# Performance work log

Measured on AMD Instinct MI355X. Metric: run time of the kernel, lower is better.

Reference implementation:

```python
import jax, jax.numpy as jnp
import numpy as np

NUM_HEADS = 16
KEY_DEPTH = 1024


def setup_inputs() -> dict:
    key = jax.random.key(0)
    ks = jax.random.split(key, 7)
    B, L, D = 2, 2048, 1024
    scale = 1.0 / np.sqrt(D)
    return {
        "query_antecedent": jax.random.normal(ks[0], (B, L, D), jnp.float32),
        "memory_antecedent": jax.random.normal(ks[1], (B, L, D), jnp.float32),
        "bias": jax.random.normal(ks[2], (1, 1, L, L), jnp.float32),
        "Wq": jax.random.normal(ks[3], (D, KEY_DEPTH), jnp.float32) * scale,
        "Wk": jax.random.normal(ks[4], (D, KEY_DEPTH), jnp.float32) * scale,
        "Wv": jax.random.normal(ks[5], (D, KEY_DEPTH), jnp.float32) * scale,
        "Wo": jax.random.normal(ks[6], (KEY_DEPTH, D), jnp.float32) * scale,
    }


def _split_heads(x, h):
    # [B, L, D] -> [B, H, L, D/H]
    b, l, d = x.shape
    return x.reshape(b, l, h, d // h).transpose(0, 2, 1, 3)


def reference(query_antecedent, memory_antecedent, bias, Wq, Wk, Wv, Wo):
    h = NUM_HEADS
    d_head = KEY_DEPTH // h
    q = _split_heads(query_antecedent @ Wq, h) * (d_head ** -0.5)
    k = _split_heads(memory_antecedent @ Wk, h)
    v = _split_heads(memory_antecedent @ Wv, h)
    # [B, H, Lq, Lk]
    logits = jnp.einsum("bhqd,bhkd->bhqk", q, k) + bias
    weights = jax.nn.softmax(logits, axis=-1)
    x = jnp.einsum("bhqk,bhkd->bhqd", weights, v)
    # combine heads: [B, H, L, d] -> [B, L, H*d]
    b, _, l, d = x.shape
    x = x.transpose(0, 2, 1, 3).reshape(b, l, h * d)
    return x @ Wo
```

## Files before the change

kernel.cpp:

```cpp
#include <hip/hip_runtime.h>
#include <hip/hip_bf16.h>


typedef __attribute__((ext_vector_type(8))) short short8;
typedef __attribute__((ext_vector_type(4))) short short4v;
typedef __attribute__((ext_vector_type(4))) float float4v;

#define BATCH 2
#define LSEQ 2048
#define DMODEL 1024
#define NHEADS 16
#define DHEAD 64
#define MROWS 4096
#define QKVLD 3072

__global__ __launch_bounds__(256)
void convert_kernel(const float* __restrict__ qa, const float* __restrict__ ma,
                    __hip_bfloat16* __restrict__ qo, __hip_bfloat16* __restrict__ mo)
{
    const size_t i = ((size_t)blockIdx.x * 256 + threadIdx.x) * 8;
    const float* src = blockIdx.y ? ma : qa;
    __hip_bfloat16* dst = blockIdx.y ? mo : qo;
    float4 v0 = *reinterpret_cast<const float4*>(src + i);
    float4 v1 = *reinterpret_cast<const float4*>(src + i + 4);
    union { __hip_bfloat16 h[8]; int4 v; } pk;
    pk.h[0] = (__hip_bfloat16)v0.x; pk.h[1] = (__hip_bfloat16)v0.y;
    pk.h[2] = (__hip_bfloat16)v0.z; pk.h[3] = (__hip_bfloat16)v0.w;
    pk.h[4] = (__hip_bfloat16)v1.x; pk.h[5] = (__hip_bfloat16)v1.y;
    pk.h[6] = (__hip_bfloat16)v1.z; pk.h[7] = (__hip_bfloat16)v1.w;
    *reinterpret_cast<int4*>(dst + i) = pk.v;
}

__global__ __launch_bounds__(256)
void transpose_w_kernel(const float* __restrict__ W0, const float* __restrict__ W1,
                        const float* __restrict__ W2, const float* __restrict__ W3,
                        __hip_bfloat16* __restrict__ T0, __hip_bfloat16* __restrict__ T1,
                        __hip_bfloat16* __restrict__ T2, __hip_bfloat16* __restrict__ T3)
{
    __shared__ __hip_bfloat16 T[64][68];

    const float* W; __hip_bfloat16* D;
    if      (blockIdx.z == 0) { W = W0; D = T0; }
    else if (blockIdx.z == 1) { W = W1; D = T1; }
    else if (blockIdx.z == 2) { W = W2; D = T2; }
    else                      { W = W3; D = T3; }

    const int t  = threadIdx.x;
    const int n0 = blockIdx.x * 64;
    const int k0 = blockIdx.y * 64;

#pragma unroll
    for (int p = 0; p < 4; ++p) {
        const int r = p * 16 + (t >> 4);
        const int c = (t & 15) * 4;
        float4 v = *reinterpret_cast<const float4*>(&W[(size_t)(k0 + r) * DMODEL + n0 + c]);
        union { __hip_bfloat16 h[4]; ushort4 v; } pk;
        pk.h[0] = (__hip_bfloat16)v.x; pk.h[1] = (__hip_bfloat16)v.y;
        pk.h[2] = (__hip_bfloat16)v.z; pk.h[3] = (__hip_bfloat16)v.w;
        *reinterpret_cast<ushort4*>(&T[r][c]) = pk.v;
    }
    __syncthreads();
#pragma unroll
    for (int p = 0; p < 2; ++p) {
        const int n  = p * 32 + (t & 31);
        const int kc = (t >> 5) * 8;
        union { __hip_bfloat16 h[8]; int4 v; } pk;
#pragma unroll
        for (int j = 0; j < 8; ++j) pk.h[j] = T[kc + j][n];
        *reinterpret_cast<int4*>(&D[(size_t)(n0 + n) * DMODEL + k0 + kc]) = pk.v;
    }
}

__global__ __launch_bounds__(256)
void gemm_bt_kernel(const __hip_bfloat16* __restrict__ A0,
                    const __hip_bfloat16* __restrict__ A1, int nsplit,
                    float alpha0, float alpha1,
                    const __hip_bfloat16* __restrict__ Bt,
                    float* __restrict__ Cf, __hip_bfloat16* __restrict__ Cb,
                    int K, int ldc)
{
    __shared__ __hip_bfloat16 As[128][40];
    __shared__ __hip_bfloat16 Bs[128][40];

    const int t    = threadIdx.x;
    const int w    = t >> 6;
    const int lane = t & 63;
    const int l15  = lane & 15;
    const int lq   = lane >> 4;
    const int m0   = blockIdx.y * 128;
    const int n0   = blockIdx.x * 128;
    const int wm   = (w >> 1) * 64;
    const int wn   = (w & 1) * 64;
    const int sr   = t >> 1;
    const int sc   = (t & 1) * 16;

    const __hip_bfloat16* A = (n0 < nsplit) ? A0 : A1;
    const float alpha = (n0 < nsplit) ? alpha0 : alpha1;

    float4v acc[4][4];
#pragma unroll
    for (int mi = 0; mi < 4; ++mi)
#pragma unroll
        for (int ni = 0; ni < 4; ++ni) acc[mi][ni] = (float4v){0.f, 0.f, 0.f, 0.f};

    const __hip_bfloat16* Arow = A  + (size_t)(m0 + sr) * K + sc;
    const __hip_bfloat16* Brow = Bt + (size_t)(n0 + sr) * K + sc;

    int4 a0 = *reinterpret_cast<const int4*>(Arow);
    int4 a1 = *reinterpret_cast<const int4*>(Arow + 8);
    int4 b0 = *reinterpret_cast<const int4*>(Brow);
    int4 b1 = *reinterpret_cast<const int4*>(Brow + 8);

    for (int k0 = 0; k0 < K; k0 += 32) {
        __syncthreads();
        *reinterpret_cast<int4*>(&As[sr][sc])     = a0;
        *reinterpret_cast<int4*>(&As[sr][sc + 8]) = a1;
        *reinterpret_cast<int4*>(&Bs[sr][sc])     = b0;
        *reinterpret_cast<int4*>(&Bs[sr][sc + 8]) = b1;
        const int kn = (k0 + 32 < K) ? k0 + 32 : k0;
        a0 = *reinterpret_cast<const int4*>(Arow + kn);
        a1 = *reinterpret_cast<const int4*>(Arow + kn + 8);
        b0 = *reinterpret_cast<const int4*>(Brow + kn);
        b1 = *reinterpret_cast<const int4*>(Brow + kn + 8);
        __syncthreads();

        short8 af[4], bf[4];
#pragma unroll
        for (int mi = 0; mi < 4; ++mi)
            af[mi] = *reinterpret_cast<const short8*>(&As[wm + mi * 16 + l15][lq * 8]);
#pragma unroll
        for (int ni = 0; ni < 4; ++ni)
            bf[ni] = *reinterpret_cast<const short8*>(&Bs[wn + ni * 16 + l15][lq * 8]);
#pragma unroll
        for (int mi = 0; mi < 4; ++mi)
#pragma unroll
            for (int ni = 0; ni < 4; ++ni)
                acc[mi][ni] = __builtin_amdgcn_mfma_f32_16x16x32_bf16(
                    af[mi], bf[ni], acc[mi][ni], 0, 0, 0);
    }

#pragma unroll
    for (int mi = 0; mi < 4; ++mi)
#pragma unroll
        for (int ni = 0; ni < 4; ++ni)
#pragma unroll
            for (int r = 0; r < 4; ++r) {
                const int row = m0 + wm + mi * 16 + lq * 4 + r;
                const int col = n0 + wn + ni * 16 + l15;
                const float v = acc[mi][ni][r] * alpha;
                if (Cf) Cf[(size_t)row * ldc + col] = v;
                else    Cb[(size_t)row * ldc + col] = (__hip_bfloat16)v;
            }
}

#define KSTR 68
#define PSTR 132

__global__ __launch_bounds__(512, 4)
void attn_mfma_kernel(const __hip_bfloat16* __restrict__ QKV,
                      const float* __restrict__ bias,
                      __hip_bfloat16* __restrict__ X)
{
    __shared__ __hip_bfloat16 Ks[128][KSTR];
    __shared__ __hip_bfloat16 Vt[64][PSTR];

    const int t   = threadIdx.x;
    const int w   = t >> 6;
    const int l15 = t & 15;
    const int lq  = (t & 63) >> 4;

    const int bid = blockIdx.x;
    const int r8  = bid & 7;
    const int j   = bid >> 3;
    const int bh  = r8 + 8 * (j >> 4);
    const int q0  = (j & 15) * 128;
    const int b   = bh >> 4;
    const int h   = bh & 15;

    const __hip_bfloat16* Kb = QKV + (size_t)b * LSEQ * QKVLD + 1024 + h * DHEAD;
    const __hip_bfloat16* Vb = Kb + 1024;

    short8 aq[2];
    {
        const __hip_bfloat16* qrow = QKV +
            (size_t)(b * LSEQ + q0 + w * 16 + l15) * QKVLD + h * DHEAD + lq * 8;
        aq[0] = *reinterpret_cast<const short8*>(qrow);
        aq[1] = *reinterpret_cast<const short8*>(qrow + 32);
    }

    const float* bp = bias + (size_t)(q0 + w * 16 + l15) * LSEQ + lq * 4;

    float lsum = 0.f;
    float4v o_acc[4];
#pragma unroll
    for (int n = 0; n < 4; ++n) o_acc[n] = (float4v){0.f, 0.f, 0.f, 0.f};

    const int skey = t >> 2;
    const int sdh  = (t & 3) * 16;
    const int a    = t & 3;
    const int cblk = ((skey >> 5) << 2) | ((skey >> 2) & 3);
    const int vcol = (((cblk ^ a) << 3)) | ((((skey >> 4) & 1) << 2)) | (skey & 3);

    int4 pk0, pk1, pv0, pv1;
    {
        const __hip_bfloat16* ks = Kb + (size_t)skey * QKVLD + sdh;
        pk0 = *reinterpret_cast<const int4*>(ks);
        pk1 = *reinterpret_cast<const int4*>(ks + 8);
        const __hip_bfloat16* vs = Vb + (size_t)skey * QKVLD + sdh;
        pv0 = *reinterpret_cast<const int4*>(vs);
        pv1 = *reinterpret_cast<const int4*>(vs + 8);
    }

    for (int kt = 0; kt < LSEQ / 128; ++kt) {
        const int k0 = kt * 128;
        __syncthreads();
        *reinterpret_cast<int4*>(&Ks[skey][sdh])     = pk0;
        *reinterpret_cast<int4*>(&Ks[skey][sdh + 8]) = pk1;
        {
            const __hip_bfloat16* vp0 = reinterpret_cast<const __hip_bfloat16*>(&pv0);
            const __hip_bfloat16* vp1 = reinterpret_cast<const __hip_bfloat16*>(&pv1);
#pragma unroll
            for (int jj = 0; jj < 8; ++jj) Vt[sdh + jj][vcol]     = vp0[jj];
#pragma unroll
            for (int jj = 0; jj < 8; ++jj) Vt[sdh + 8 + jj][vcol] = vp1[jj];
        }
        {
            const int knext = (kt + 1 < LSEQ / 128) ? k0 + 128 : k0;
            const __hip_bfloat16* ks = Kb + (size_t)(knext + skey) * QKVLD + sdh;
            pk0 = *reinterpret_cast<const int4*>(ks);
            pk1 = *reinterpret_cast<const int4*>(ks + 8);
            const __hip_bfloat16* vs = Vb + (size_t)(knext + skey) * QKVLD + sdh;
            pv0 = *reinterpret_cast<const int4*>(vs);
            pv1 = *reinterpret_cast<const int4*>(vs + 8);
        }
        __syncthreads();

#pragma unroll
        for (int m = 0; m < 4; ++m) {
            short8 bkA0 = *reinterpret_cast<const short8*>(&Ks[(2*m)    *16 + l15][lq * 8]);
            short8 bkA1 = *reinterpret_cast<const short8*>(&Ks[(2*m)    *16 + l15][32 + lq * 8]);
            short8 bkB0 = *reinterpret_cast<const short8*>(&Ks[(2*m + 1)*16 + l15][lq * 8]);
            short8 bkB1 = *reinterpret_cast<const short8*>(&Ks[(2*m + 1)*16 + l15][32 + lq * 8]);
            float4v bvA = *reinterpret_cast<const float4v*>(bp + k0 + 32 * m);
            float4v bvB = *reinterpret_cast<const float4v*>(bp + k0 + 32 * m + 16);

            float4v sA = (float4v){0.f, 0.f, 0.f, 0.f};
            float4v sB = (float4v){0.f, 0.f, 0.f, 0.f};
            __builtin_amdgcn_s_setprio(1);
            sA = __builtin_amdgcn_mfma_f32_16x16x32_bf16(bkA0, aq[0], sA, 0, 0, 0);
            sA = __builtin_amdgcn_mfma_f32_16x16x32_bf16(bkA1, aq[1], sA, 0, 0, 0);
            sB = __builtin_amdgcn_mfma_f32_16x16x32_bf16(bkB0, aq[0], sB, 0, 0, 0);
            sB = __builtin_amdgcn_mfma_f32_16x16x32_bf16(bkB1, aq[1], sB, 0, 0, 0);
            __builtin_amdgcn_s_setprio(0);

            union { __hip_bfloat16 hh[8]; short8 v; } pp;
#pragma unroll
            for (int r = 0; r < 4; ++r) {
                const float e = __expf(sA[r] + bvA[r]);
                lsum += e;
                pp.hh[r] = (__hip_bfloat16)e;
            }
#pragma unroll
            for (int r = 0; r < 4; ++r) {
                const float e = __expf(sB[r] + bvB[r]);
                lsum += e;
                pp.hh[4 + r] = (__hip_bfloat16)e;
            }
            const short8 pf = pp.v;

            short8 vt[4];
#pragma unroll
            for (int n = 0; n < 4; ++n)
                vt[n] = *reinterpret_cast<const short8*>(
                    &Vt[n * 16 + l15][((m * 4 + lq) ^ n) << 3]);

            __builtin_amdgcn_s_setprio(1);
#pragma unroll
            for (int n = 0; n < 4; ++n)
                o_acc[n] = __builtin_amdgcn_mfma_f32_16x16x32_bf16(
                    vt[n], pf, o_acc[n], 0, 0, 0);
            __builtin_amdgcn_s_setprio(0);
        }
    }

    lsum += __shfl_xor(lsum, 16);
    lsum += __shfl_xor(lsum, 32);
    const float inv = 1.f / lsum;
    {
        const int row = q0 + w * 16 + l15;
        __hip_bfloat16* dst = X + (size_t)(b * LSEQ + row) * DMODEL + h * DHEAD + lq * 4;
#pragma unroll
        for (int n = 0; n < 4; ++n) {
            union { __hip_bfloat16 hh[4]; short4v v; } o;
#pragma unroll
            for (int r = 0; r < 4; ++r) o.hh[r] = (__hip_bfloat16)(o_acc[n][r] * inv);
            *reinterpret_cast<short4v*>(dst + n * 16) = o.v;
        }
    }
}

extern "C" void kernel_launch(void* const* d_in, const int* in_sizes, int n_in,
                              void* d_out, int out_size, void* d_ws, size_t ws_size,
                              hipStream_t stream)
{
    const float* qa   = (const float*)d_in[0];
    const float* ma   = (const float*)d_in[1];
    const float* bias = (const float*)d_in[2];
    const float* Wq   = (const float*)d_in[3];
    const float* Wk   = (const float*)d_in[4];
    const float* Wv   = (const float*)d_in[5];
    const float* Wo   = (const float*)d_in[6];
    float* out = (float*)d_out;

    char* wsb = (char*)d_ws;
    __hip_bfloat16* qa16 = (__hip_bfloat16*)(wsb);
    __hip_bfloat16* ma16 = (__hip_bfloat16*)(wsb + (8u << 20));
    __hip_bfloat16* Wt   = (__hip_bfloat16*)(wsb + (16u << 20));
    __hip_bfloat16* Wot  = (__hip_bfloat16*)(wsb + (22u << 20));
    __hip_bfloat16* QKVw = (__hip_bfloat16*)(wsb + (24u << 20));
    __hip_bfloat16* Xw   = qa16;

    convert_kernel<<<dim3(MROWS * DMODEL / (256 * 8), 2), 256, 0, stream>>>(
        qa, ma, qa16, ma16);

    transpose_w_kernel<<<dim3(16, 16, 4), 256, 0, stream>>>(
        Wq, Wk, Wv, Wo,
        Wt, Wt + (size_t)DMODEL * DMODEL, Wt + 2 * (size_t)DMODEL * DMODEL, Wot);

    gemm_bt_kernel<<<dim3(QKVLD / 128, MROWS / 128), 256, 0, stream>>>(
        qa16, ma16, DMODEL, 0.125f, 1.0f, Wt, nullptr, QKVw, DMODEL, QKVLD);

    attn_mfma_kernel<<<dim3(512), 512, 0, stream>>>(QKVw, bias, Xw);

    gemm_bt_kernel<<<dim3(DMODEL / 128, MROWS / 128), 256, 0, stream>>>(
        Xw, Xw, DMODEL + 1, 1.0f, 1.0f, Wot, out, nullptr, DMODEL, DMODEL);
}
```

Measured before the change: 246.0 us.

## Use direct global-to-LDS loads, BK=64 swizzled tiles, and XCD-aware block mapping in GEMM

The GEMM kernel now stages A/B tiles with global_load_lds straight into LDS, using a 64-wide K tile with an XOR swizzle in place of padding, instead of register-prefetched stores. A 1D grid is remapped so each of the 8 XCD groups gets contiguous M rows for L2 reuse, and launch bounds request 2 blocks per CU. The attention kernel's V-transpose swizzle is also changed to shift the XOR key. The aim is to cut register staging and LDS bank conflicts, but the loop waits on vmcnt(0) with no double buffering, so load latency is no longer overlapped with MFMA work.

```diff
diff --git a/kernel.cpp b/kernel.cpp
--- a/kernel.cpp
+++ b/kernel.cpp
@@ -71,72 +71,86 @@
     }
 }
 
-__global__ __launch_bounds__(256)
+#define GBK 64
+
+__global__ __launch_bounds__(256, 2)
 void gemm_bt_kernel(const __hip_bfloat16* __restrict__ A0,
                     const __hip_bfloat16* __restrict__ A1, int nsplit,
                     float alpha0, float alpha1,
                     const __hip_bfloat16* __restrict__ Bt,
                     float* __restrict__ Cf, __hip_bfloat16* __restrict__ Cb,
-                    int K, int ldc)
-{
-    __shared__ __hip_bfloat16 As[128][40];
-    __shared__ __hip_bfloat16 Bs[128][40];
+                    int K, int ldc, int nbx)
+{
+    __shared__ __hip_bfloat16 As[128][GBK];
+    __shared__ __hip_bfloat16 Bs[128][GBK];
 
     const int t    = threadIdx.x;
     const int w    = t >> 6;
     const int lane = t & 63;
     const int l15  = lane & 15;
     const int lq   = lane >> 4;
-    const int m0   = blockIdx.y * 128;
-    const int n0   = blockIdx.x * 128;
     const int wm   = (w >> 1) * 64;
     const int wn   = (w & 1) * 64;
-    const int sr   = t >> 1;
-    const int sc   = (t & 1) * 16;
+
+    const int nwg  = gridDim.x;
+    const int c    = blockIdx.x & 7;
+    const int q    = blockIdx.x >> 3;
+    const int mper = (nwg >> 3) / nbx;
+    const int m0   = (c * mper + q / nbx) * 128;
+    const int n0   = (q % nbx) * 128;
 
     const __hip_bfloat16* A = (n0 < nsplit) ? A0 : A1;
     const float alpha = (n0 < nsplit) ? alpha0 : alpha1;
 
+    const int lrow = lane >> 3;
+    const int lch  = (lane & 7) ^ lrow;
+
     float4v acc[4][4];
 #pragma unroll
     for (int mi = 0; mi < 4; ++mi)
 #pragma unroll
         for (int ni = 0; ni < 4; ++ni) acc[mi][ni] = (float4v){0.f, 0.f, 0.f, 0.f};
 
-    const __hip_bfloat16* Arow = A  + (size_t)(m0 + sr) * K + sc;
-    const __hip_bfloat16* Brow = Bt + (size_t)(n0 + sr) * K + sc;
-
-    int4 a0 = *reinterpret_cast<const int4*>(Arow);
-    int4 a1 = *reinterpret_cast<const int4*>(Arow + 8);
-    int4 b0 = *reinterpret_cast<const int4*>(Brow);
-    int4 b1 = *reinterpret_cast<const int4*>(Brow + 8);
-
-    for (int k0 = 0; k0 < K; k0 += 32) {
+    for (int k0 = 0; k0 < K; k0 += GBK) {
         __syncthreads();
-        *reinterpret_cast<int4*>(&As[sr][sc])     = a0;
-        *reinterpret_cast<int4*>(&As[sr][sc + 8]) = a1;
-        *reinterpret_cast<int4*>(&Bs[sr][sc])     = b0;
-        *reinterpret_cast<int4*>(&Bs[sr][sc + 8]) = b1;
-        const int kn = (k0 + 32 < K) ? k0 + 32 : k0;
-        a0 = *reinterpret_cast<const int4*>(Arow + kn);
-        a1 = *reinterpret_cast<const int4*>(Arow + kn + 8);
-        b0 = *reinterpret_cast<const int4*>(Brow + kn);
-        b1 = *reinterpret_cast<const int4*>(Brow + kn + 8);
+#pragma unroll
+        for (int i = 0; i < 4; ++i) {
+            const int rb = (w * 4 + i) * 8;
+            const int r  = rb + lrow;
+            __builtin_amdgcn_global_load_lds(
+                (const __attribute__((address_space(1))) void*)
+                    (A + (size_t)(m0 + r) * K + k0 + lch * 8),
+                (__attribute__((address_space(3))) void*)&As[rb][0], 16, 0, 0);
+            __builtin_amdgcn_global_load_lds(
+                (const __attribute__((address_space(1))) void*)
+                    (Bt + (size_t)(n0 + r) * K + k0 + lch * 8),
+                (__attribute__((address_space(3))) void*)&Bs[rb][0], 16, 0, 0);
+        }
+        asm volatile("s_waitcnt vmcnt(0)" ::: "memory");
         __syncthreads();
 
-        short8 af[4], bf[4];
-#pragma unroll
-        for (int mi = 0; mi < 4; ++mi)
-            af[mi] = *reinterpret_cast<const short8*>(&As[wm + mi * 16 + l15][lq * 8]);
-#pragma unroll
-        for (int ni = 0; ni < 4; ++ni)
-            bf[ni] = *reinterpret_cast<const short8*>(&Bs[wn + ni * 16 + l15][lq * 8]);
-#pragma unroll
-        for (int mi = 0; mi < 4; ++mi)
-#pragma unroll
-            for (int ni = 0; ni < 4; ++ni)
-                acc[mi][ni] = __builtin_amdgcn_mfma_f32_16x16x32_bf16(
-                    af[mi], bf[ni], acc[mi][ni], 0, 0, 0);
+#pragma unroll
+        for (int kh = 0; kh < 2; ++kh) {
+            short8 af[4], bf[4];
+#pragma unroll
+            for (int mi = 0; mi < 4; ++mi) {
+                const int r = wm + mi * 16 + l15;
+                af[mi] = *reinterpret_cast<const short8*>(
+                    &As[r][(((kh << 2) | lq) ^ (r & 7)) << 3]);
+            }
+#pragma unroll
+            for (int ni = 0; ni < 4; ++ni) {
+                const int r = wn + ni * 16 + l15;
+                bf[ni] = *reinterpret_cast<const short8*>(
+                    &Bs[r][(((kh << 2) | lq) ^ (r & 7)) << 3]);
+            }
+#pragma unroll
+            for (int mi = 0; mi < 4; ++mi)
+#pragma unroll
+                for (int ni = 0; ni < 4; ++ni)
+                    acc[mi][ni] = __builtin_amdgcn_mfma_f32_16x16x32_bf16(
+                        af[mi], bf[ni], acc[mi][ni], 0, 0, 0);
+        }
     }
 
 #pragma unroll
@@ -199,7 +213,7 @@
     const int sdh  = (t & 3) * 16;
     const int a    = t & 3;
     const int cblk = ((skey >> 5) << 2) | ((skey >> 2) & 3);
-    const int vcol = (((cblk ^ a) << 3)) | ((((skey >> 4) & 1) << 2)) | (skey & 3);
+    const int vcol = (((cblk ^ (a << 2)) << 3)) | ((((skey >> 4) & 1) << 2)) | (skey & 3);
 
     int4 pk0, pk1, pv0, pv1;
     {
@@ -272,7 +286,7 @@
 #pragma unroll
             for (int n = 0; n < 4; ++n)
                 vt[n] = *reinterpret_cast<const short8*>(
-                    &Vt[n * 16 + l15][((m * 4 + lq) ^ n) << 3]);
+                    &Vt[n * 16 + l15][((m * 4 + lq) ^ (n << 2)) << 3]);
 
             __builtin_amdgcn_s_setprio(1);
 #pragma unroll
@@ -327,11 +341,11 @@
         Wq, Wk, Wv, Wo,
         Wt, Wt + (size_t)DMODEL * DMODEL, Wt + 2 * (size_t)DMODEL * DMODEL, Wot);
 
-    gemm_bt_kernel<<<dim3(QKVLD / 128, MROWS / 128), 256, 0, stream>>>(
-        qa16, ma16, DMODEL, 0.125f, 1.0f, Wt, nullptr, QKVw, DMODEL, QKVLD);
+    gemm_bt_kernel<<<dim3(768), 256, 0, stream>>>(
+        qa16, ma16, DMODEL, 0.125f, 1.0f, Wt, nullptr, QKVw, DMODEL, QKVLD, 24);
 
     attn_mfma_kernel<<<dim3(512), 512, 0, stream>>>(QKVw, bias, Xw);
 
-    gemm_bt_kernel<<<dim3(DMODEL / 128, MROWS / 128), 256, 0, stream>>>(
-        Xw, Xw, DMODEL + 1, 1.0f, 1.0f, Wot, out, nullptr, DMODEL, DMODEL);
-}
+    gemm_bt_kernel<<<dim3(256), 256, 0, stream>>>(
+        Xw, Xw, DMODEL + 1, 1.0f, 1.0f, Wot, out, nullptr, DMODEL, DMODEL, 8);
+}
```

Measured after the change: 240.8 us. 1.02x faster.
